# Performance work log

Measured on AMD Instinct MI355X. Metric: run time of the kernel, lower is better.

Reference implementation:

```python
import jax, jax.numpy as jnp
import numpy as np

HEADS = 16  # init kwarg 'heads'

def setup_inputs() -> dict:
    key = jax.random.key(0)
    k1, k2, k3 = jax.random.split(key, 3)
    B, S, D = 2, 2048, 1024
    x = jax.random.normal(k1, (B, S, D), dtype=jnp.float32)
    # nn.Linear(dim, 3*dim, bias=False): y = x @ W^T; store as [D, 3D] already transposed.
    w_qkv = jax.random.normal(k2, (D, 3 * D), dtype=jnp.float32) * 0.02
    w_out = jax.random.normal(k3, (D, D), dtype=jnp.float32) * 0.02
    return {"x": x, "w_qkv": w_qkv, "w_out": w_out}

def reference(x, w_qkv, w_out):
    B, S, D = x.shape
    H = HEADS
    hd = D // H
    scale = 1.0 / jnp.sqrt(jnp.asarray(hd, dtype=x.dtype))
    qkv = x @ w_qkv                      # [B, S, 3D]
    q, k, v = jnp.split(qkv, 3, axis=-1)
    def to_heads(t):
        return t.reshape(B, S, H, hd).transpose(0, 2, 1, 3)  # [B, H, S, hd]
    q, k, v = to_heads(q), to_heads(k), to_heads(v)
    scores = jnp.einsum('bhqd,bhkd->bhqk', q, k) * scale      # [B, H, S, S]
    # causal mask: query i attends to keys j <= i
    causal = jnp.tril(jnp.ones((S, S), dtype=bool))
    scores = jnp.where(causal, scores, -jnp.inf)
    p = jax.nn.softmax(scores, axis=-1)  # online-softmax in the original == exact softmax
    o = jnp.einsum('bhqk,bhkd->bhqd', p, v)                   # [B, H, S, hd]
    out = o.transpose(0, 2, 1, 3).reshape(B, S, D)
    return out @ w_out
```

## Files before the change

kernel.cpp:

```cpp
#include <hip/hip_runtime.h>


typedef unsigned short u16;
typedef unsigned int   u32;
typedef __attribute__((ext_vector_type(4))) u16    u16x4;
typedef __attribute__((ext_vector_type(8))) u16    u16x8;
typedef __attribute__((ext_vector_type(4))) short  s16x4;
typedef __attribute__((ext_vector_type(8))) __bf16 bf16x8;
typedef __attribute__((ext_vector_type(4))) float  f32x4;
typedef __attribute__((ext_vector_type(16))) float f32x16;

#define DEV static __device__ __forceinline__

DEV u16 f2b(float f) {
  unsigned u = __float_as_uint(f);
  u += 0x7fffu + ((u >> 16) & 1u);
  return (u16)(u >> 16);
}

DEV void gload_lds16(const void* g, void* l) {
  __builtin_amdgcn_global_load_lds((const __attribute__((address_space(1))) void*)g,
                                   (__attribute__((address_space(3))) void*)l, 16, 0, 0);
}

DEV unsigned lds_off(const void* p) {
  return (unsigned)(unsigned long long)(const __attribute__((address_space(3))) void*)p;
}

DEV s16x4 tr_read(unsigned off) {
  s16x4 d;
  asm volatile("ds_read_b64_tr_b16 %0, %1" : "=v"(d) : "v"(off));
  return d;
}

DEV u32 cvt_pk(float lo, float hi) {
  u32 r;
  asm("v_cvt_pk_bf16_f32 %0, %1, %2" : "=v"(r) : "v"(lo), "v"(hi));
  return r;
}

DEV void pswap(u32& x, u32& y) {
  asm volatile("v_permlane32_swap_b32 %0, %1" : "+v"(x), "+v"(y));
}

DEV f32x4 mfma32(bf16x8 a, bf16x8 b, f32x4 c) {
  return __builtin_amdgcn_mfma_f32_16x16x32_bf16(a, b, c, 0, 0, 0);
}
DEV f32x16 mfma3232(bf16x8 a, bf16x8 b, f32x16 c) {
  return __builtin_amdgcn_mfma_f32_32x32x16_bf16(a, b, c, 0, 0, 0);
}

__global__ __launch_bounds__(256) void cvt_kernel(const float* __restrict__ in,
                                                  u16* __restrict__ out, int n4) {
  int i = blockIdx.x * 256 + threadIdx.x;
  if (i >= n4) return;
  const float4 v = ((const float4*)in)[i];
  u16x4 o = { f2b(v.x), f2b(v.y), f2b(v.z), f2b(v.w) };
  ((u16x4*)out)[i] = o;
}

__global__ __launch_bounds__(256) void transpose_cvt(const float* __restrict__ w,
                                                     u16* __restrict__ wt,
                                                     const int Kdim, const int Ndim,
                                                     const int scaleN) {
  __shared__ u16 ls[32][33];
  const int tn = blockIdx.x * 32, tk = blockIdx.y * 32;
  const int t = threadIdx.x;
  const int r = t >> 3, c4 = (t & 7) * 4;
  const float s = (tn < scaleN) ? 0.18033688011112042f : 1.0f;
  float4 v = *(const float4*)(w + (size_t)(tk + r) * Ndim + tn + c4);
  ls[r][c4 + 0] = f2b(v.x * s); ls[r][c4 + 1] = f2b(v.y * s);
  ls[r][c4 + 2] = f2b(v.z * s); ls[r][c4 + 3] = f2b(v.w * s);
  __syncthreads();
  u16x4 ov = { ls[c4 + 0][r], ls[c4 + 1][r], ls[c4 + 2][r], ls[c4 + 3][r] };
  *(u16x4*)(wt + (size_t)(tn + r) * Kdim + tk + c4) = ov;
}

__global__ __launch_bounds__(256) void gemm_qkv(const u16* __restrict__ A,
                                                const u16* __restrict__ Bt,
                                                u16* __restrict__ C, const int ldc) {
  const int gx = gridDim.x;
  const int id = (int)(blockIdx.y * gx + blockIdx.x);
  const int nxp = gx >> 3;
  const int xcd = id & 7, loc = id >> 3;
  const int tn = (xcd * nxp + loc % nxp) * 128;
  const int tm = (loc / nxp) * 128;
  const int tid = threadIdx.x;
  const int wave = tid >> 6, lane = tid & 63;
  const int wr = wave >> 1, wc = wave & 1;
  const int lg = lane >> 4, lc = lane & 15;
  __shared__ __align__(128) u16 lsA[128 * 64];
  __shared__ __align__(128) u16 lsB[128 * 64];

  f32x4 acc[4][4];
#pragma unroll
  for (int i = 0; i < 4; ++i)
#pragma unroll
    for (int j = 0; j < 4; ++j) acc[i][j] = (f32x4){0.f, 0.f, 0.f, 0.f};

  for (int kt = 0; kt < 16; ++kt) {
#pragma unroll
    for (int c = 0; c < 4; ++c) {
      const int p = tid + c * 256;
      const int row = p >> 3, ck = p & 7;
      const int cg = ck ^ (row & 7);
      gload_lds16(A  + (size_t)(tm + row) * 1024 + kt * 64 + cg * 8, (char*)lsA + p * 16);
      gload_lds16(Bt + (size_t)(tn + row) * 1024 + kt * 64 + cg * 8, (char*)lsB + p * 16);
    }
    __syncthreads();
#pragma unroll
    for (int kk = 0; kk < 2; ++kk) {
      bf16x8 af[4], bg[4];
#pragma unroll
      for (int i = 0; i < 4; ++i) {
        const int ar = wr * 64 + i * 16 + lc;
        af[i] = *(const bf16x8*)(lsA + ar * 64 + ((kk * 4 + lg) ^ (ar & 7)) * 8);
        const int br = wc * 64 + i * 16 + lc;
        bg[i] = *(const bf16x8*)(lsB + br * 64 + ((kk * 4 + lg) ^ (br & 7)) * 8);
      }
#pragma unroll
      for (int i = 0; i < 4; ++i)
#pragma unroll
        for (int j = 0; j < 4; ++j)
          acc[i][j] = mfma32(af[i], bg[j], acc[i][j]);
    }
    __syncthreads();
  }

#pragma unroll
  for (int i = 0; i < 4; ++i) {
#pragma unroll
    for (int r = 0; r < 4; ++r) {
      const int m = tm + wr * 64 + i * 16 + lg * 4 + r;
#pragma unroll
      for (int j = 0; j < 4; ++j) {
        const int n = tn + wc * 64 + j * 16 + lc;
        C[(size_t)m * ldc + n] = f2b(acc[i][j][r]);
      }
    }
  }
}

__global__ __launch_bounds__(256) void gemm_bt64(const u16* __restrict__ A,
                                                 const u16* __restrict__ Bt,
                                                 float* __restrict__ C, const int ldc) {
  const int id = (int)(blockIdx.y * 8 + blockIdx.x);
  const int tn = (id & 7) * 128;
  const int tm = (id >> 3) * 64;
  const int tid = threadIdx.x;
  const int wave = tid >> 6, lane = tid & 63;
  const int wc = wave;
  const int lg = lane >> 4, lc = lane & 15;
  __shared__ __align__(128) u16 lsA[64 * 32];
  __shared__ __align__(128) u16 lsB[128 * 32];

  f32x4 acc[4][2];
#pragma unroll
  for (int i = 0; i < 4; ++i)
#pragma unroll
    for (int j = 0; j < 2; ++j) acc[i][j] = (f32x4){0.f, 0.f, 0.f, 0.f};

  for (int kt = 0; kt < 32; ++kt) {
    {
      const int p = tid;
      const int row = p >> 2, ck = p & 3;
      const int cg = ck ^ ((row >> 1) & 3);
      gload_lds16(A + (size_t)(tm + row) * 1024 + kt * 32 + cg * 8, (char*)lsA + p * 16);
    }
#pragma unroll
    for (int c = 0; c < 2; ++c) {
      const int p = tid + c * 256;
      const int row = p >> 2, ck = p & 3;
      const int cg = ck ^ ((row >> 1) & 3);
      gload_lds16(Bt + (size_t)(tn + row) * 1024 + kt * 32 + cg * 8, (char*)lsB + p * 16);
    }
    __syncthreads();
    bf16x8 af[4], bg[2];
#pragma unroll
    for (int i = 0; i < 4; ++i) {
      const int ar = i * 16 + lc;
      af[i] = *(const bf16x8*)(lsA + ar * 32 + (lg ^ ((ar >> 1) & 3)) * 8);
    }
#pragma unroll
    for (int j = 0; j < 2; ++j) {
      const int br = wc * 32 + j * 16 + lc;
      bg[j] = *(const bf16x8*)(lsB + br * 32 + (lg ^ ((br >> 1) & 3)) * 8);
    }
#pragma unroll
    for (int i = 0; i < 4; ++i)
#pragma unroll
      for (int j = 0; j < 2; ++j)
        acc[i][j] = mfma32(af[i], bg[j], acc[i][j]);
    __syncthreads();
  }

#pragma unroll
  for (int i = 0; i < 4; ++i) {
#pragma unroll
    for (int r = 0; r < 4; ++r) {
      const int m = tm + i * 16 + lg * 4 + r;
#pragma unroll
      for (int j = 0; j < 2; ++j) {
        const int n = tn + wc * 32 + j * 16 + lc;
        C[(size_t)m * ldc + n] = acc[i][j][r];
      }
    }
  }
}

__global__ __launch_bounds__(128, 2) void attn_kernel(const u16* __restrict__ qkv,
                                                      u16* __restrict__ o) {
  const int qb  = 63 - (int)(blockIdx.x >> 5);
  const int bh  = blockIdx.x & 31;
  const int b   = bh >> 4, h = bh & 15;
  const int tid  = threadIdx.x;
  const int wave = tid >> 6, lane = tid & 63;
  const int l31 = lane & 31, lg2 = lane >> 5;

  __shared__ __align__(128) char smem[2][8192];
  __shared__ float lsm[2][32];
  char* wb = smem[wave];
  const unsigned vb = lds_off(wb + 4096);

  const size_t bS = (size_t)b * 2048;
  const int T  = qb + 1;
  const int q0 = qb * 32;

  const u16* qrow = qkv + (bS + q0 + l31) * 3072 + h * 64;
  bf16x8 qf[4];
#pragma unroll
  for (int m = 0; m < 4; ++m)
    qf[m] = *(const bf16x8*)(qrow + 16 * m + 8 * lg2);

  unsigned koff[4], voff[4];
#pragma unroll
  for (int c = 0; c < 4; ++c) {
    const int p = c * 64 + lane;
    {
      const int row = p >> 3;
      const int cg = (p & 7) ^ (row & 7);
      koff[c] = (unsigned)(row * 3072 + 1024 + h * 64 + cg * 8);
    }
    {
      const int s = p >> 3, cw = p & 7;
      voff[c] = (unsigned)((4 * (s >> 2) + (cw >> 1)) * 3072 + 2048 + h * 64
                           + (s & 3) * 16 + (cw & 1) * 8);
    }
  }

  auto STAGE = [&](int t) {
    const u16* base = qkv + (bS + (size_t)t * 32) * 3072;
#pragma unroll
    for (int c = 0; c < 4; ++c)
      gload_lds16(base + koff[c], wb + (c * 64 + lane) * 16);
#pragma unroll
    for (int c = 0; c < 4; ++c)
      gload_lds16(base + voff[c], wb + 4096 + (c * 64 + lane) * 16);
  };

  float lsum = 0.f;
  f32x16 accO[2];
#pragma unroll
  for (int r = 0; r < 16; ++r) { accO[0][r] = 0.f; accO[1][r] = 0.f; }

  if (wave < T) STAGE(wave);

  for (int t = wave; t < T; t += 2) {
    asm volatile("s_waitcnt vmcnt(0)" ::: "memory");
    __builtin_amdgcn_sched_barrier(0);

    const u16* kbp = (const u16*)wb + l31 * 64;
    bf16x8 kf[4];
#pragma unroll
    for (int m = 0; m < 4; ++m)
      kf[m] = *(const bf16x8*)(kbp + (((2 * m + lg2) ^ (l31 & 7)) * 8));
    s16x4 vr[2][2][2];
#pragma unroll
    for (int db = 0; db < 2; ++db)
#pragma unroll
      for (int hh = 0; hh < 2; ++hh) {
        const unsigned a0 = vb +
          (unsigned)(((4 * hh + 2 * lg2) * 4 + db * 2 + (l31 >> 4)) * 128 + (l31 & 15) * 8);
        vr[db][hh][0] = tr_read(a0);
        vr[db][hh][1] = tr_read(a0 + 512);
      }
    asm volatile("s_waitcnt lgkmcnt(0)" ::: "memory");
    __builtin_amdgcn_sched_barrier(0);

    if (t + 2 < T) STAGE(t + 2);
    __builtin_amdgcn_sched_barrier(0);

    f32x16 sc;
#pragma unroll
    for (int r = 0; r < 16; ++r) sc[r] = 0.f;
    __builtin_amdgcn_s_setprio(1);
#pragma unroll
    for (int m = 0; m < 4; ++m)
      sc = mfma3232(kf[m], qf[m], sc);
    __builtin_amdgcn_s_setprio(0);

    float pp[16];
    if (t == T - 1) {
#pragma unroll
      for (int r = 0; r < 16; ++r) {
        const int kvp = (r & 3) + 8 * (r >> 2) + 4 * lg2;
        pp[r] = (kvp <= l31) ? exp2f(sc[r]) : 0.f;
      }
    } else {
#pragma unroll
      for (int r = 0; r < 16; ++r) pp[r] = exp2f(sc[r]);
    }
#pragma unroll
    for (int r = 0; r < 16; ++r) lsum += pp[r];

    u32 a01 = cvt_pk(pp[0], pp[1]),   a23 = cvt_pk(pp[2], pp[3]);
    u32 b01 = cvt_pk(pp[4], pp[5]),   b23 = cvt_pk(pp[6], pp[7]);
    u32 c01 = cvt_pk(pp[8], pp[9]),   c23 = cvt_pk(pp[10], pp[11]);
    u32 d01 = cvt_pk(pp[12], pp[13]), d23 = cvt_pk(pp[14], pp[15]);
    pswap(a01, b01); pswap(a23, b23);
    pswap(c01, d01); pswap(c23, d23);
    union Frag { u32 w[4]; bf16x8 v; };
    Frag f0, f1;
    f0.w[0] = a01; f0.w[1] = a23; f0.w[2] = b01; f0.w[3] = b23;
    f1.w[0] = c01; f1.w[1] = c23; f1.w[2] = d01; f1.w[3] = d23;

    __builtin_amdgcn_s_setprio(1);
#pragma unroll
    for (int db = 0; db < 2; ++db) {
      union { s16x4 hh[2]; bf16x8 v; } u0, u1;
      u0.hh[0] = vr[db][0][0]; u0.hh[1] = vr[db][0][1];
      u1.hh[0] = vr[db][1][0]; u1.hh[1] = vr[db][1][1];
      accO[db] = mfma3232(f0.v, u0.v, accO[db]);
      accO[db] = mfma3232(f1.v, u1.v, accO[db]);
    }
    __builtin_amdgcn_s_setprio(0);
  }

  lsum += __shfl_xor(lsum, 32);
  float* mO = (float*)wb;
#pragma unroll
  for (int db = 0; db < 2; ++db)
#pragma unroll
    for (int r = 0; r < 16; ++r) {
      const int qp = (r & 3) + 8 * (r >> 2) + 4 * lg2;
      mO[qp * 64 + db * 32 + l31] = accO[db][r];
    }
  if (lane < 32) lsm[wave][l31] = lsum;
  __syncthreads();

  const float* O0 = (const float*)smem[0];
  const float* O1 = (const float*)smem[1];
  const int q  = wave * 16 + (lane >> 2);
  const int d0 = (lane & 3) * 16;
  const float inv = 1.f / (lsm[0][q] + lsm[1][q]);
  u16x8 ov[2];
#pragma unroll
  for (int j = 0; j < 4; ++j) {
    const f32x4 a = *(const f32x4*)(O0 + q * 64 + d0 + j * 4);
    const f32x4 c = *(const f32x4*)(O1 + q * 64 + d0 + j * 4);
#pragma unroll
    for (int e = 0; e < 4; ++e)
      ov[j >> 1][(j & 1) * 4 + e] = f2b((a[e] + c[e]) * inv);
  }
  const size_t orow = (bS + q0 + q) * 1024 + h * 64 + d0;
  *(u16x8*)(o + orow)     = ov[0];
  *(u16x8*)(o + orow + 8) = ov[1];
}

extern "C" void kernel_launch(void* const* d_in, const int* in_sizes, int n_in,
                              void* d_out, int out_size, void* d_ws, size_t ws_size,
                              hipStream_t stream) {
  const float* x     = (const float*)d_in[0];
  const float* w_qkv = (const float*)d_in[1];
  const float* w_out = (const float*)d_in[2];
  float* out = (float*)d_out;
  char* ws = (char*)d_ws;

  u16* xb    = (u16*)(ws + 0);
  u16* wqkvT = (u16*)(ws + 8388608);
  u16* woutT = (u16*)(ws + 14680064);
  u16* qkvb  = (u16*)(ws + 16777216);
  u16* ob    = (u16*)(ws + 41943040);

  cvt_kernel<<<4096, 256, 0, stream>>>(x, xb, 1048576);
  transpose_cvt<<<dim3(96, 32), 256, 0, stream>>>(w_qkv, wqkvT, 1024, 3072, 1024);
  transpose_cvt<<<dim3(32, 32), 256, 0, stream>>>(w_out, woutT, 1024, 1024, 0);
  gemm_qkv<<<dim3(24, 32), 256, 0, stream>>>(xb, wqkvT, qkvb, 3072);
  attn_kernel<<<2048, 128, 0, stream>>>(qkvb, ob);
  gemm_bt64<<<dim3(8, 64), 256, 0, stream>>>(ob, woutT, out, 1024);
}
```

Measured before the change: 105.6 us.

## Split attention KV loop across four waves per block instead of two

Each attention block now runs four waves, each taking every fourth KV tile, which shortens the per-block serial KV loop, especially for late causal query blocks. Partial outputs are reduced through shared memory in two stages, with even waves writing and odd waves accumulating, before normalisation and bf16 store. This doubles per-block LDS and thread count, which may reduce co-resident blocks. It also adds extra barriers and leaves waves idle on early query blocks that have few KV tiles.

```diff
diff --git a/kernel.cpp b/kernel.cpp
--- a/kernel.cpp
+++ b/kernel.cpp
@@ -208,7 +208,7 @@
   }
 }
 
-__global__ __launch_bounds__(128, 2) void attn_kernel(const u16* __restrict__ qkv,
+__global__ __launch_bounds__(256, 2) void attn_kernel(const u16* __restrict__ qkv,
                                                       u16* __restrict__ o) {
   const int qb  = 63 - (int)(blockIdx.x >> 5);
   const int bh  = blockIdx.x & 31;
@@ -217,8 +217,8 @@
   const int wave = tid >> 6, lane = tid & 63;
   const int l31 = lane & 31, lg2 = lane >> 5;
 
-  __shared__ __align__(128) char smem[2][8192];
-  __shared__ float lsm[2][32];
+  __shared__ __align__(128) char smem[4][8192];
+  __shared__ float lsm[4][32];
   char* wb = smem[wave];
   const unsigned vb = lds_off(wb + 4096);
 
@@ -265,7 +265,7 @@
 
   if (wave < T) STAGE(wave);
 
-  for (int t = wave; t < T; t += 2) {
+  for (int t = wave; t < T; t += 4) {
     asm volatile("s_waitcnt vmcnt(0)" ::: "memory");
     __builtin_amdgcn_sched_barrier(0);
 
@@ -287,7 +287,7 @@
     asm volatile("s_waitcnt lgkmcnt(0)" ::: "memory");
     __builtin_amdgcn_sched_barrier(0);
 
-    if (t + 2 < T) STAGE(t + 2);
+    if (t + 4 < T) STAGE(t + 4);
     __builtin_amdgcn_sched_barrier(0);
 
     f32x16 sc;
@@ -337,34 +337,41 @@
   }
 
   lsum += __shfl_xor(lsum, 32);
-  float* mO = (float*)wb;
-#pragma unroll
-  for (int db = 0; db < 2; ++db)
-#pragma unroll
-    for (int r = 0; r < 16; ++r) {
-      const int qp = (r & 3) + 8 * (r >> 2) + 4 * lg2;
-      mO[qp * 64 + db * 32 + l31] = accO[db][r];
-    }
   if (lane < 32) lsm[wave][l31] = lsum;
+  float* mA = (float*)smem[0];
+  float* mB = (float*)smem[2];
   __syncthreads();
-
-  const float* O0 = (const float*)smem[0];
-  const float* O1 = (const float*)smem[1];
-  const int q  = wave * 16 + (lane >> 2);
-  const int d0 = (lane & 3) * 16;
-  const float inv = 1.f / (lsm[0][q] + lsm[1][q]);
-  u16x8 ov[2];
-#pragma unroll
-  for (int j = 0; j < 4; ++j) {
-    const f32x4 a = *(const f32x4*)(O0 + q * 64 + d0 + j * 4);
-    const f32x4 c = *(const f32x4*)(O1 + q * 64 + d0 + j * 4);
-#pragma unroll
-    for (int e = 0; e < 4; ++e)
-      ov[j >> 1][(j & 1) * 4 + e] = f2b((a[e] + c[e]) * inv);
-  }
-  const size_t orow = (bS + q0 + q) * 1024 + h * 64 + d0;
-  *(u16x8*)(o + orow)     = ov[0];
-  *(u16x8*)(o + orow + 8) = ov[1];
+  if ((wave & 1) == 0) {
+    float* m = (wave == 0) ? mA : mB;
+#pragma unroll
+    for (int db = 0; db < 2; ++db)
+#pragma unroll
+      for (int r = 0; r < 16; ++r) {
+        const int qp = (r & 3) + 8 * (r >> 2) + 4 * lg2;
+        m[qp * 64 + db * 32 + l31] = accO[db][r];
+      }
+  }
+  __syncthreads();
+  if ((wave & 1) == 1) {
+    float* m = (wave == 1) ? mA : mB;
+#pragma unroll
+    for (int db = 0; db < 2; ++db)
+#pragma unroll
+      for (int r = 0; r < 16; ++r) {
+        const int qp = (r & 3) + 8 * (r >> 2) + 4 * lg2;
+        m[qp * 64 + db * 32 + l31] += accO[db][r];
+      }
+  }
+  __syncthreads();
+
+  const int q  = tid >> 3;
+  const int d0 = (tid & 7) * 8;
+  const float inv = 1.f / (lsm[0][q] + lsm[1][q] + lsm[2][q] + lsm[3][q]);
+  u16x8 ov;
+#pragma unroll
+  for (int e = 0; e < 8; ++e)
+    ov[e] = f2b((mA[q * 64 + d0 + e] + mB[q * 64 + d0 + e]) * inv);
+  *(u16x8*)(o + (bS + q0 + q) * 1024 + h * 64 + d0) = ov;
 }
 
 extern "C" void kernel_launch(void* const* d_in, const int* in_sizes, int n_in,
@@ -386,6 +393,6 @@
   transpose_cvt<<<dim3(96, 32), 256, 0, stream>>>(w_qkv, wqkvT, 1024, 3072, 1024);
   transpose_cvt<<<dim3(32, 32), 256, 0, stream>>>(w_out, woutT, 1024, 1024, 0);
   gemm_qkv<<<dim3(24, 32), 256, 0, stream>>>(xb, wqkvT, qkvb, 3072);
-  attn_kernel<<<2048, 128, 0, stream>>>(qkvb, ob);
+  attn_kernel<<<2048, 256, 0, stream>>>(qkvb, ob);
   gemm_bt64<<<dim3(8, 64), 256, 0, stream>>>(ob, woutT, out, 1024);
 }
```

Result: no change. 105.5 us (-0.1%).
